# Performance work log

Measured on AMD Instinct MI355X. Metric: run time of the kernel, lower is better.

The kernel has to match this reference:

```python
import jax, jax.numpy as jnp
import numpy as np

D_MODEL = 2048
N_HEADS = 16
D_HEAD = 128
BATCH = 2
SEQ = 2048


def setup_inputs() -> dict:
    key = jax.random.key(0)
    ks = jax.random.split(key, 5)
    x = jax.random.normal(ks[0], (BATCH, SEQ, D_MODEL), dtype=jnp.float32)
    # fused QKV projection: out features = d_model + 2*d_head
    W_qkv = jax.random.normal(ks[1], (D_MODEL, D_MODEL + 2 * D_HEAD), dtype=jnp.float32) * (D_MODEL ** -0.5)
    b_qkv = jax.random.normal(ks[2], (D_MODEL + 2 * D_HEAD,), dtype=jnp.float32) * 0.02
    W_out = jax.random.normal(ks[3], (D_MODEL, D_MODEL), dtype=jnp.float32) * (D_MODEL ** -0.5)
    b_out = jax.random.normal(ks[4], (D_MODEL,), dtype=jnp.float32) * 0.02
    return {"x": x, "W_qkv": W_qkv, "b_qkv": b_qkv, "W_out": W_out, "b_out": b_out}


def reference(x, W_qkv, b_qkv, W_out, b_out):
    B, S, _ = x.shape
    qkv = jnp.einsum('bsd,de->bse', x, W_qkv) + b_qkv
    q, k, v = jnp.split(qkv, [D_MODEL, D_MODEL + D_HEAD], axis=-1)
    # q: [B, H, S, Dh]; k, v: single shared head [B, S, Dh] (MQA broadcast)
    q = q.reshape(B, S, N_HEADS, D_HEAD).transpose(0, 2, 1, 3)
    scale = 1.0 / jnp.sqrt(jnp.float32(D_HEAD))
    # scores: [B, H, S, S] -- shared K broadcast across heads
    scores = jnp.einsum('bhqd,bkd->bhqk', q, k) * scale
    causal = jnp.tril(jnp.ones((S, S), dtype=bool))
    scores = jnp.where(causal, scores, jnp.finfo(scores.dtype).min)
    attn = jax.nn.softmax(scores, axis=-1)
    out = jnp.einsum('bhqk,bkd->bhqd', attn, v)  # shared V broadcast
    out = out.transpose(0, 2, 1, 3).reshape(B, S, D_MODEL)
    return jnp.einsum('bsd,de->bse', out, W_out) + b_out
```

## Files before the change

### kernel.cpp

```cpp
#include <hip/hip_runtime.h>

#define D_MODEL 2048
#define QKVC 2304
#define DH 128
#define NH 16
#define BATCH 2
#define SEQ 2048
#define MROWS (BATCH*SEQ)

typedef __attribute__((ext_vector_type(4))) float f32x4;
typedef __attribute__((ext_vector_type(16))) float f32x16;
typedef __attribute__((ext_vector_type(8))) short s16x8;
typedef __attribute__((ext_vector_type(8))) __bf16 bf16x8;
typedef __attribute__((ext_vector_type(4))) unsigned int u32x4;

static __device__ __forceinline__ unsigned short f2bf(float f) {
  unsigned int u = __builtin_bit_cast(unsigned int, f);
  u += 0x7fff + ((u >> 16) & 1);
  return (unsigned short)(u >> 16);
}

static __device__ __forceinline__ float bf2f(unsigned short s) {
  unsigned int u = ((unsigned int)s) << 16;
  return __builtin_bit_cast(float, u);
}

static __device__ __forceinline__ unsigned int pkbf(float a, float b) {
  unsigned short x = __builtin_bit_cast(unsigned short, (__bf16)a);
  unsigned short y = __builtin_bit_cast(unsigned short, (__bf16)b);
  return (unsigned int)x | ((unsigned int)y << 16);
}

static __device__ __forceinline__ f32x4 mfma16(s16x8 a, s16x8 b, f32x4 c) {
  return __builtin_amdgcn_mfma_f32_16x16x32_bf16(
      __builtin_bit_cast(bf16x8, a), __builtin_bit_cast(bf16x8, b), c, 0, 0, 0);
}

static __device__ __forceinline__ f32x16 mfma32(s16x8 a, s16x8 b, f32x16 c) {
  return __builtin_amdgcn_mfma_f32_32x32x16_bf16(
      __builtin_bit_cast(bf16x8, a), __builtin_bit_cast(bf16x8, b), c, 0, 0, 0);
}

typedef const __attribute__((address_space(1))) void gvoid_t;
typedef __attribute__((address_space(3))) void svoid_t;

static __device__ __forceinline__ void gload_lds16(const void* g, void* l) {
  __builtin_amdgcn_global_load_lds((gvoid_t*)g, (svoid_t*)l, 16, 0, 0);
}

__global__ void cvt_bf16_kernel(const float* __restrict__ in,
                                unsigned short* __restrict__ out, int n4) {
  int i = blockIdx.x * blockDim.x + threadIdx.x;
  int stride = gridDim.x * blockDim.x;
  for (int idx = i; idx < n4; idx += stride) {
    float4 v = ((const float4*)in)[idx];
    ushort4 o;
    o.x = f2bf(v.x); o.y = f2bf(v.y); o.z = f2bf(v.z); o.w = f2bf(v.w);
    ((ushort4*)out)[idx] = o;
  }
}

__global__ void transpose_cvt_kernel(const float* __restrict__ in,
                                     unsigned short* __restrict__ out,
                                     int R, int C) {
  __shared__ float tile[32][33];
  int c0 = blockIdx.x * 32, r0 = blockIdx.y * 32;
  int tx = threadIdx.x, ty = threadIdx.y;
#pragma unroll
  for (int i = 0; i < 4; ++i)
    tile[ty + i*8][tx] = in[(size_t)(r0 + ty + i*8) * C + c0 + tx];
  __syncthreads();
#pragma unroll
  for (int i = 0; i < 4; ++i)
    out[(size_t)(c0 + ty + i*8) * R + r0 + tx] = f2bf(tile[tx][ty + i*8]);
}

__global__ void transpose_v_kernel(const unsigned short* __restrict__ qkv,
                                   unsigned short* __restrict__ VT) {
  __shared__ unsigned short tile[32][33];
  int s0 = blockIdx.x * 32, d0 = blockIdx.y * 32, b = blockIdx.z;
  int tx = threadIdx.x, ty = threadIdx.y;
#pragma unroll
  for (int i = 0; i < 4; ++i)
    tile[ty + i*8][tx] =
        qkv[(size_t)(b*SEQ + s0 + ty + i*8) * QKVC + (D_MODEL + DH) + d0 + tx];
  __syncthreads();
#pragma unroll
  for (int i = 0; i < 4; ++i)
    VT[(size_t)(b*DH + d0 + ty + i*8) * SEQ + s0 + tx] = tile[tx][ty + i*8];
}

template<int OUT_F32>
__global__ __launch_bounds__(256, 2)
void gemm_bt_kernel(const unsigned short* __restrict__ A,
                    const unsigned short* __restrict__ BT,
                    const float* __restrict__ bias,
                    void* __restrict__ Cout,
                    int M, int N, int K) {
  __shared__ unsigned short Al[128*32];
  __shared__ unsigned short Bl[128*32];
  int tid = threadIdx.x;
  int lane = tid & 63, wave = tid >> 6;
  int m0 = blockIdx.y * 128, n0 = blockIdx.x * 128;
  int wr = wave >> 1, wc = wave & 1;
  int fr = lane & 15, fq = lane >> 4;
  f32x4 acc[4][4] = {};

  int c0 = wave * 2;
  int kcol = (lane & 3) * 8;
  int rsub = (lane >> 2);

  for (int k0 = 0; k0 < K; k0 += 32) {
#pragma unroll
    for (int i = 0; i < 2; ++i) {
      int c = c0 + i;
      int row = c*16 + rsub;
      gload_lds16(A  + (size_t)(m0 + row)*K + k0 + kcol, (char*)Al + c*1024);
      gload_lds16(BT + (size_t)(n0 + row)*K + k0 + kcol, (char*)Bl + c*1024);
    }
    __syncthreads();
    s16x8 af[4], bfr[4];
#pragma unroll
    for (int m = 0; m < 4; ++m)
      af[m] = *(const s16x8*)&Al[(wr*64 + m*16 + fr)*32 + fq*8];
#pragma unroll
    for (int n = 0; n < 4; ++n)
      bfr[n] = *(const s16x8*)&Bl[(wc*64 + n*16 + fr)*32 + fq*8];
#pragma unroll
    for (int m = 0; m < 4; ++m)
#pragma unroll
      for (int n = 0; n < 4; ++n)
        acc[m][n] = mfma16(af[m], bfr[n], acc[m][n]);
    __syncthreads();
  }

#pragma unroll
  for (int n = 0; n < 4; ++n) {
    int col = n0 + wc*64 + n*16 + fr;
    float bv = bias[col];
#pragma unroll
    for (int m = 0; m < 4; ++m) {
      int rowb = m0 + wr*64 + m*16 + fq*4;
#pragma unroll
      for (int j = 0; j < 4; ++j) {
        float v = acc[m][n][j] + bv;
        if (OUT_F32) ((float*)Cout)[(size_t)(rowb + j)*N + col] = v;
        else ((unsigned short*)Cout)[(size_t)(rowb + j)*N + col] = f2bf(v);
      }
    }
  }
}

__global__ __launch_bounds__(256, 2)
void mqa_attn_kernel(const unsigned short* __restrict__ qkv,
                     const unsigned short* __restrict__ VT,
                     unsigned short* __restrict__ O,
                     unsigned short* __restrict__ Opart,
                     float* __restrict__ Lpart) {
  __shared__ unsigned short Kl[2][64*128];
  __shared__ unsigned short Vl[2][128*64];
  int u = blockIdx.x;
  int half = u & 1;
  int x  = (u >> 1) & 31;
  int hg = (u >> 6) & 3;
  int b  = u >> 8;
  int qtA = 63 - x, qtB = x;
  int nkbB = (qtB >> 1) + 1;

  int tid = threadIdx.x;
  int lane = tid & 63;
  int wid = tid >> 6;
  int fr = lane & 31, hi = lane >> 5;
  int h = hg*4 + wid;
  const float C  = 0.12751688f;
  const float mC = 17.312340490667560f;

  int n_items = half ? 16 : 17;

#define ITEM_OF(i_, qt_, kb_) do {                                          \
    if (!half)            { qt_ = qtA; kb_ = (i_); }                        \
    else if ((i_) < nkbB) { qt_ = qtB; kb_ = (i_); }                        \
    else                  { qt_ = qtA; kb_ = 17 + (i_) - nkbB; }            \
  } while (0)

#define STAGE(kb_, buf_) do {                                               \
    int kv0_ = (kb_)*64;                                                    \
    _Pragma("unroll")                                                       \
    for (int i_ = 0; i_ < 4; ++i_) {                                        \
      int idx_ = i_*256 + tid;                                              \
      int r_ = idx_ >> 4, c_ = idx_ & 15;                                   \
      gload_lds16(qkv + (size_t)(b*SEQ + kv0_ + r_)*QKVC + D_MODEL          \
                      + ((c_ ^ (r_ & 15)) * 8),                             \
                  (char*)&Kl[buf_][0] + (size_t)idx_*16);                   \
      int d_ = idx_ >> 3, c2_ = idx_ & 7;                                   \
      gload_lds16(VT + (size_t)(b*DH + d_)*SEQ + kv0_ + ((c2_^(d_&7))*8),   \
                  (char*)&Vl[buf_][0] + (size_t)idx_*16);                   \
    }                                                                       \
  } while (0)

  s16x8 qf[8];
  f32x16 oacc[4];
  float l_r;

  auto load_q = [&](int qt_) {
    const unsigned short* qb =
        qkv + (size_t)(b*SEQ + qt_*32 + fr)*QKVC + h*DH + hi*8;
#pragma unroll
    for (int s = 0; s < 8; ++s) qf[s] = *(const s16x8*)(qb + s*16);
  };
  auto reset_state = [&]() {
#pragma unroll
    for (int n2 = 0; n2 < 4; ++n2)
#pragma unroll
      for (int e = 0; e < 16; ++e) oacc[n2][e] = 0.f;
    l_r = 0.f;
  };

  auto do_tile = [&](const unsigned short* Kb, const unsigned short* Vb,
                     int q0, int kv0) {
    f32x16 sfr[2] = {};
    __builtin_amdgcn_s_setprio(1);
#pragma unroll
    for (int t = 0; t < 2; ++t) {
      int row = t*32 + fr;
#pragma unroll
      for (int s = 0; s < 8; ++s) {
        int cc = (s*2 + hi) ^ (fr & 15);
        s16x8 kf = *(const s16x8*)&Kb[row*128 + cc*8];
        sfr[t] = mfma32(kf, qf[s], sfr[t]);
      }
    }
    __builtin_amdgcn_s_setprio(0);

    if (kv0 + 63 > q0) {
      int q = q0 + fr;
#pragma unroll
      for (int t = 0; t < 2; ++t)
#pragma unroll
        for (int r = 0; r < 16; ++r) {
          int kv = kv0 + t*32 + (r & 3) + 8*(r >> 2) + 4*hi;
          if (kv > q) sfr[t][r] = -1.0e30f;
        }
    }

    float rs = 0.f;
#pragma unroll
    for (int t = 0; t < 2; ++t)
#pragma unroll
      for (int r = 0; r < 16; ++r) {
        float p = exp2f(__builtin_fmaf(sfr[t][r], C, -mC));
        sfr[t][r] = p;
        rs += p;
      }
    rs += __shfl_xor(rs, 32);
    l_r += rs;

#pragma unroll
    for (int t = 0; t < 2; ++t) {
      s16x8 pa[2];
#pragma unroll
      for (int ks = 0; ks < 2; ++ks) {
        unsigned int X0 = pkbf(sfr[t][8*ks+0], sfr[t][8*ks+1]);
        unsigned int X1 = pkbf(sfr[t][8*ks+2], sfr[t][8*ks+3]);
        unsigned int Y0 = pkbf(sfr[t][8*ks+4], sfr[t][8*ks+5]);
        unsigned int Y1 = pkbf(sfr[t][8*ks+6], sfr[t][8*ks+7]);
        unsigned int s0 = __shfl_xor(hi ? X0 : Y0, 32);
        unsigned int s1 = __shfl_xor(hi ? X1 : Y1, 32);
        u32x4 pw;
        pw[0] = hi ? s0 : X0;
        pw[1] = hi ? s1 : X1;
        pw[2] = hi ? Y0 : s0;
        pw[3] = hi ? Y1 : s1;
        pa[ks] = __builtin_bit_cast(s16x8, pw);
      }
      __builtin_amdgcn_s_setprio(1);
#pragma unroll
      for (int n2 = 0; n2 < 4; ++n2) {
        int d = n2*32 + fr;
#pragma unroll
        for (int ks = 0; ks < 2; ++ks) {
          int cc = (t*4 + ks*2 + hi) ^ (d & 7);
          s16x8 vf = *(const s16x8*)&Vb[d*64 + cc*8];
          oacc[n2] = mfma32(pa[ks], vf, oacc[n2]);
        }
      }
      __builtin_amdgcn_s_setprio(0);
    }
  };

  auto do_epilogue = [&](int qt_) {
    float invl = 1.0f / l_r;
#pragma unroll
    for (int r = 0; r < 16; ++r) {
      int qrow = (r & 3) + 8*(r >> 2) + 4*hi;
      float iv = __shfl(invl, qrow);
      size_t rowoff = (size_t)(b*SEQ + qt_*32 + qrow)*D_MODEL + h*DH;
#pragma unroll
      for (int n2 = 0; n2 < 4; ++n2)
        O[rowoff + n2*32 + fr] = f2bf(oacc[n2][r] * iv);
    }
  };

  load_q(half ? qtB : qtA);
  reset_state();

  {
    int qt0, kb0; ITEM_OF(0, qt0, kb0);
    STAGE(kb0, 0);
  }
  __syncthreads();

  for (int i = 0; i < n_items; ++i) {
    if (i + 1 < n_items) {
      int qtn, kbn; ITEM_OF(i + 1, qtn, kbn);
      STAGE(kbn, (i + 1) & 1);
    }
    int qtc, kbc; ITEM_OF(i, qtc, kbc);
    do_tile(&Kl[i & 1][0], &Vl[i & 1][0], qtc*32, kbc*64);
    if (half && i == nkbB - 1) {
      do_epilogue(qtB);
      load_q(qtA);
      reset_state();
    }
    __syncthreads();
  }

  {
    size_t pbase = ((size_t)u*4 + wid)*32;
#pragma unroll
    for (int r = 0; r < 16; ++r) {
      int q = (r & 3) + 8*(r >> 2) + 4*hi;
#pragma unroll
      for (int n2 = 0; n2 < 4; ++n2)
        Opart[(pbase + q)*128 + n2*32 + fr] = f2bf(oacc[n2][r]);
    }
    if (hi == 0) Lpart[pbase + fr] = l_r;
  }
#undef STAGE
#undef ITEM_OF
}

__global__ __launch_bounds__(256)
void attn_merge_kernel(const unsigned short* __restrict__ Opart,
                       const float* __restrict__ Lpart,
                       unsigned short* __restrict__ O) {
  int m = blockIdx.x;
  int x = m & 31, hg = (m >> 5) & 3, b = m >> 7;
  int qtA = 63 - x;
  int w = threadIdx.x >> 6;
  int lane = threadIdx.x & 63;
  int h = hg*4 + w;
  size_t r0 = ((size_t)(m*2 + 0)*4 + w)*32;
  size_t r1 = ((size_t)(m*2 + 1)*4 + w)*32;
  int d = lane * 2;
#pragma unroll 4
  for (int q = 0; q < 32; ++q) {
    float inv = 1.0f / (Lpart[r0 + q] + Lpart[r1 + q]);
    float o0 = bf2f(Opart[(r0+q)*128 + d])     + bf2f(Opart[(r1+q)*128 + d]);
    float o1 = bf2f(Opart[(r0+q)*128 + d + 1]) + bf2f(Opart[(r1+q)*128 + d + 1]);
    size_t off = (size_t)(b*SEQ + qtA*32 + q)*D_MODEL + h*DH + d;
    O[off]     = f2bf(o0 * inv);
    O[off + 1] = f2bf(o1 * inv);
  }
}

extern "C" void kernel_launch(void* const* d_in, const int* in_sizes, int n_in,
                              void* d_out, int out_size, void* d_ws, size_t ws_size,
                              hipStream_t stream) {
  const float* x     = (const float*)d_in[0];
  const float* W_qkv = (const float*)d_in[1];
  const float* b_qkv = (const float*)d_in[2];
  const float* W_out = (const float*)d_in[3];
  const float* b_out = (const float*)d_in[4];
  float* out = (float*)d_out;

  unsigned short* x_bf = (unsigned short*)d_ws;
  unsigned short* WqT  = x_bf + (size_t)MROWS * D_MODEL;
  unsigned short* WoT  = WqT  + (size_t)QKVC * D_MODEL;
  unsigned short* qkvb = WoT  + (size_t)D_MODEL * D_MODEL;
  unsigned short* VTb  = qkvb + (size_t)MROWS * QKVC;
  unsigned short* Ob   = VTb  + (size_t)BATCH * DH * SEQ;

  unsigned short* Opart = x_bf;
  float* Lpart = (float*)WqT;

  dim3 tb(32, 8);
  cvt_bf16_kernel<<<2048, 256, 0, stream>>>(x, x_bf, (MROWS * D_MODEL) / 4);
  transpose_cvt_kernel<<<dim3(QKVC/32, D_MODEL/32), tb, 0, stream>>>(W_qkv, WqT, D_MODEL, QKVC);
  transpose_cvt_kernel<<<dim3(D_MODEL/32, D_MODEL/32), tb, 0, stream>>>(W_out, WoT, D_MODEL, D_MODEL);

  gemm_bt_kernel<0><<<dim3(QKVC/128, MROWS/128), 256, 0, stream>>>(
      x_bf, WqT, b_qkv, qkvb, MROWS, QKVC, D_MODEL);

  transpose_v_kernel<<<dim3(SEQ/32, DH/32, BATCH), tb, 0, stream>>>(qkvb, VTb);

  mqa_attn_kernel<<<dim3(512), 256, 0, stream>>>(qkvb, VTb, Ob, Opart, Lpart);
  attn_merge_kernel<<<dim3(256), 256, 0, stream>>>(Opart, Lpart, Ob);

  gemm_bt_kernel<1><<<dim3(D_MODEL/128, MROWS/128), 256, 0, stream>>>(
      Ob, WoT, b_out, out, MROWS, D_MODEL, D_MODEL);
}
```

Before: 201.2 us.

## Vectorize weight transpose, raise GEMM occupancy hint, precompute attention stage pointers

The weight transpose-convert kernel now uses 64x64 tiles, with float4 loads and ushort4 stores, to cut the number of memory transactions. The GEMM launch bound goes from 2 to 3 waves per SIMD, which may force register spills. The attention kernel's K/V staging now advances precomputed per-thread pointers instead of recomputing swizzled addresses each iteration, and jumps by a fixed stride when a half-block switches query tiles. The shared-memory transpose reads with a padded 65-column stride may have some bank conflicts on the vectorized read side.

New measurement: 194.5 us. 1.03x faster.

```diff
diff --git a/kernel.cpp b/kernel.cpp
--- a/kernel.cpp
+++ b/kernel.cpp
@@ -63,16 +63,28 @@
 __global__ void transpose_cvt_kernel(const float* __restrict__ in,
                                      unsigned short* __restrict__ out,
                                      int R, int C) {
-  __shared__ float tile[32][33];
-  int c0 = blockIdx.x * 32, r0 = blockIdx.y * 32;
-  int tx = threadIdx.x, ty = threadIdx.y;
-#pragma unroll
-  for (int i = 0; i < 4; ++i)
-    tile[ty + i*8][tx] = in[(size_t)(r0 + ty + i*8) * C + c0 + tx];
+  __shared__ float tile[64][65];
+  int c0 = blockIdx.x * 64, r0 = blockIdx.y * 64;
+  int tx = threadIdx.x & 15, ty = threadIdx.x >> 4;
+#pragma unroll
+  for (int i = 0; i < 4; ++i) {
+    float4 v = *(const float4*)&in[(size_t)(r0 + ty + i*16) * C + c0 + tx*4];
+    tile[ty + i*16][tx*4+0] = v.x;
+    tile[ty + i*16][tx*4+1] = v.y;
+    tile[ty + i*16][tx*4+2] = v.z;
+    tile[ty + i*16][tx*4+3] = v.w;
+  }
   __syncthreads();
 #pragma unroll
-  for (int i = 0; i < 4; ++i)
-    out[(size_t)(c0 + ty + i*8) * R + r0 + tx] = f2bf(tile[tx][ty + i*8]);
+  for (int i = 0; i < 4; ++i) {
+    int c = ty + i*16;
+    ushort4 o;
+    o.x = f2bf(tile[tx*4+0][c]);
+    o.y = f2bf(tile[tx*4+1][c]);
+    o.z = f2bf(tile[tx*4+2][c]);
+    o.w = f2bf(tile[tx*4+3][c]);
+    *(ushort4*)&out[(size_t)(c0 + c) * R + r0 + tx*4] = o;
+  }
 }
 
 __global__ void transpose_v_kernel(const unsigned short* __restrict__ qkv,
@@ -91,7 +103,7 @@
 }
 
 template<int OUT_F32>
-__global__ __launch_bounds__(256, 2)
+__global__ __launch_bounds__(256, 3)
 void gemm_bt_kernel(const unsigned short* __restrict__ A,
                     const unsigned short* __restrict__ BT,
                     const float* __restrict__ bias,
@@ -159,6 +171,7 @@
                      float* __restrict__ Lpart) {
   __shared__ unsigned short Kl[2][64*128];
   __shared__ unsigned short Vl[2][128*64];
+  const int BUFB = 64*128*2;
   int u = blockIdx.x;
   int half = u & 1;
   int x  = (u >> 1) & 31;
@@ -183,18 +196,22 @@
     else                  { qt_ = qtA; kb_ = 17 + (i_) - nkbB; }            \
   } while (0)
 
-#define STAGE(kb_, buf_) do {                                               \
-    int kv0_ = (kb_)*64;                                                    \
+  const unsigned short* kptr =
+      qkv + (size_t)(b*SEQ + (tid >> 4))*QKVC + D_MODEL
+          + (((tid & 15) ^ ((tid >> 4) & 15)) * 8);
+  const unsigned short* vptr =
+      VT + (size_t)(b*DH + (tid >> 3))*SEQ
+         + (((tid & 7) ^ ((tid >> 3) & 7)) * 8);
+  const size_t KSTEP = (size_t)64 * QKVC;
+  const size_t VSTEP = 64;
+  char* kl_dst = (char*)&Kl[0][0] + (size_t)tid * 16;
+  char* vl_dst = (char*)&Vl[0][0] + (size_t)tid * 16;
+
+#define STAGE(buf_) do {                                                    \
     _Pragma("unroll")                                                       \
     for (int i_ = 0; i_ < 4; ++i_) {                                        \
-      int idx_ = i_*256 + tid;                                              \
-      int r_ = idx_ >> 4, c_ = idx_ & 15;                                   \
-      gload_lds16(qkv + (size_t)(b*SEQ + kv0_ + r_)*QKVC + D_MODEL          \
-                      + ((c_ ^ (r_ & 15)) * 8),                             \
-                  (char*)&Kl[buf_][0] + (size_t)idx_*16);                   \
-      int d_ = idx_ >> 3, c2_ = idx_ & 7;                                   \
-      gload_lds16(VT + (size_t)(b*DH + d_)*SEQ + kv0_ + ((c2_^(d_&7))*8),   \
-                  (char*)&Vl[buf_][0] + (size_t)idx_*16);                   \
+      gload_lds16(kptr + (size_t)i_*16*QKVC, kl_dst + (buf_)*BUFB + i_*4096); \
+      gload_lds16(vptr + (size_t)i_*32*SEQ,  vl_dst + (buf_)*BUFB + i_*4096); \
     }                                                                       \
   } while (0)
 
@@ -304,16 +321,16 @@
   load_q(half ? qtB : qtA);
   reset_state();
 
-  {
-    int qt0, kb0; ITEM_OF(0, qt0, kb0);
-    STAGE(kb0, 0);
-  }
+  STAGE(0);
   __syncthreads();
 
   for (int i = 0; i < n_items; ++i) {
     if (i + 1 < n_items) {
-      int qtn, kbn; ITEM_OF(i + 1, qtn, kbn);
-      STAGE(kbn, (i + 1) & 1);
+      size_t step = 1;
+      if (half && (i + 1) == nkbB) step = (size_t)(18 - nkbB);
+      kptr += step * KSTEP;
+      vptr += step * VSTEP;
+      STAGE((i + 1) & 1);
     }
     int qtc, kbc; ITEM_OF(i, qtc, kbc);
     do_tile(&Kl[i & 1][0], &Vl[i & 1][0], qtc*32, kbc*64);
@@ -384,14 +401,14 @@
   unsigned short* Opart = x_bf;
   float* Lpart = (float*)WqT;
 
-  dim3 tb(32, 8);
   cvt_bf16_kernel<<<2048, 256, 0, stream>>>(x, x_bf, (MROWS * D_MODEL) / 4);
-  transpose_cvt_kernel<<<dim3(QKVC/32, D_MODEL/32), tb, 0, stream>>>(W_qkv, WqT, D_MODEL, QKVC);
-  transpose_cvt_kernel<<<dim3(D_MODEL/32, D_MODEL/32), tb, 0, stream>>>(W_out, WoT, D_MODEL, D_MODEL);
+  transpose_cvt_kernel<<<dim3(QKVC/64, D_MODEL/64), 256, 0, stream>>>(W_qkv, WqT, D_MODEL, QKVC);
+  transpose_cvt_kernel<<<dim3(D_MODEL/64, D_MODEL/64), 256, 0, stream>>>(W_out, WoT, D_MODEL, D_MODEL);
 
   gemm_bt_kernel<0><<<dim3(QKVC/128, MROWS/128), 256, 0, stream>>>(
       x_bf, WqT, b_qkv, qkvb, MROWS, QKVC, D_MODEL);
 
+  dim3 tb(32, 8);
   transpose_v_kernel<<<dim3(SEQ/32, DH/32, BATCH), tb, 0, stream>>>(qkvb, VTb);
 
   mqa_attn_kernel<<<dim3(512), 256, 0, stream>>>(qkvb, VTb, Ob, Opart, Lpart);
```
